# Optimization experiments

Measured on AMD Instinct MI355X. Metric: run time of the kernel, lower is better.

Reference implementation:

```python
import jax, jax.numpy as jnp
import numpy as np

N_POINTS = 131072
WIDTH = 256
DEPTH = 6          # number of hidden layers
MU = 1.0
K_COND = 0.5


def setup_inputs() -> dict:
    key = jax.random.key(0)
    ks = jax.random.split(key, 2 * (DEPTH + 1) + 1)
    xyt = jax.random.uniform(ks[0], (N_POINTS, 3), dtype=jnp.float32)
    dims = [3] + [WIDTH] * DEPTH + [1]
    inp = {"xyt": xyt}
    for i in range(DEPTH + 1):
        inp[f"w{i}"] = jax.random.normal(ks[1 + i], (dims[i], dims[i + 1]), dtype=jnp.float32) / np.sqrt(dims[i]).astype(np.float32)
        inp[f"b{i}"] = jnp.zeros((dims[i + 1],), dtype=jnp.float32)
    return inp


def reference(xyt, w0, b0, w1, b1, w2, b2, w3, b3, w4, b4, w5, b5, w6, b6):
    Ws = [w0, w1, w2, w3, w4, w5, w6]
    bs = [b0, b1, b2, b3, b4, b5, b6]

    def h_fn(p):  # p: (3,) -> scalar h(x,y,t)
        z = p
        for W, b in zip(Ws[:-1], bs[:-1]):
            z = jnp.tanh(z @ W + b)
        return (z @ Ws[-1] + bs[-1])[0]

    grad_h = jax.grad(h_fn)
    ex = jnp.array([1.0, 0.0, 0.0], dtype=xyt.dtype)
    ey = jnp.array([0.0, 1.0, 0.0], dtype=xyt.dtype)

    def point(p):
        h, g = jax.value_and_grad(h_fn)(p)          # h, (h_x, h_y, h_t)
        hxx = jax.jvp(grad_h, (p,), (ex,))[1][0]    # fwd-over-rev HVP, x-direction
        hyy = jax.jvp(grad_h, (p,), (ey,))[1][1]    # fwd-over-rev HVP, y-direction
        return h, g[0], g[1], g[2], hxx, hyy

    h, hx, hy, ht, hxx, hyy = jax.vmap(point)(xyt)  # each (n,)

    x, y, t = xyt[:, 0], xyt[:, 1], xyt[:, 2]
    f = jnp.sin(jnp.pi * x) * jnp.sin(jnp.pi * y) * jnp.exp(-t)  # problem.f

    res = MU * ht - K_COND * (h * (hxx + hyy) + hx * hx + hy * hy) - f
    return res[:, None]  # (n, 1)
```

## Files before the change

kernel.cpp:

```cpp
#include <hip/hip_runtime.h>
#include <math.h>

#define WIDTH 256
#define PTS 16
#define CPLANE 20480

typedef _Float16 f16x8 __attribute__((ext_vector_type(8)));
typedef _Float16 f16x4 __attribute__((ext_vector_type(4)));
typedef __fp16   h16x2 __attribute__((ext_vector_type(2)));
typedef float    f32x4 __attribute__((ext_vector_type(4)));

__device__ __forceinline__ void split2(float f, _Float16& h, _Float16& l) {
    h = (_Float16)f;
    l = (_Float16)(f - (float)h);
}
__device__ __forceinline__ void tanh_s(float u, float& z, float& s) {
    const float t = __expf(-2.0f * fabsf(u));
    const float r = __builtin_amdgcn_rcpf(1.0f + t);
    const float zm = (1.0f - t) * r;
    z = copysignf(zm, u);
    s = 4.0f * t * r * r;
}

__global__ void prep_w_kernel(const float* __restrict__ w1, const float* __restrict__ w2,
                              const float* __restrict__ w3, const float* __restrict__ w4,
                              const float* __restrict__ w5, _Float16* __restrict__ wt2)
{
    const int idx = blockIdx.x * blockDim.x + threadIdx.x;
    if (idx >= 5 * 16 * 8 * 64) return;
    const int lane = idx & 63;
    const int kc   = (idx >> 6) & 7;
    const int jt   = (idx >> 9) & 15;
    const int l    = idx >> 13;
    const float* Wsrc[5] = { w1, w2, w3, w4, w5 };
    const float* W = Wsrc[l];
    const int j  = jt * 16 + (lane & 15);
    const int k0 = kc * 32 + (lane >> 4) * 8;
    f16x8 vh, vl;
    #pragma unroll
    for (int i = 0; i < 8; ++i) {
        _Float16 h, lo;
        split2(W[(k0 + i) * WIDTH + j], h, lo);
        vh[i] = h; vl[i] = lo;
    }
    const int fo = ((jt * 8 + kc) * 64 + lane) * 8;
    *(f16x8*)(wt2 + (l * 2 + 0) * 65536 + fo) = vh;
    *(f16x8*)(wt2 + (l * 2 + 1) * 65536 + fo) = vl;
}

__global__ __launch_bounds__(256, 2)
void pde_mfma_kernel(const float* __restrict__ xyt,
                     const float* __restrict__ w0, const float* __restrict__ b0,
                     const float* __restrict__ b1, const float* __restrict__ b2,
                     const float* __restrict__ b3, const float* __restrict__ b4,
                     const float* __restrict__ b5,
                     const float* __restrict__ w6, const float* __restrict__ b6,
                     const _Float16* __restrict__ wt2,
                     float* __restrict__ out)
{
    __shared__ _Float16 Zs[CPLANE];
    float* redf = (float*)Zs;

    const int tid = threadIdx.x;
    const long gp0 = (long)blockIdx.x * PTS;

    {
        const int p = tid & 15;
        const float x = xyt[(gp0 + p) * 3 + 0];
        const float y = xyt[(gp0 + p) * 3 + 1];
        const float t = xyt[(gp0 + p) * 3 + 2];
        #pragma unroll
        for (int half = 0; half < 2; ++half) {
            const int jg = (tid >> 4) + half * 16;
            f16x8 vh[5];
            #pragma unroll
            for (int c = 0; c < 8; ++c) {
                const int j = jg * 8 + c;
                const float wx = w0[0 * WIDTH + j];
                const float wy = w0[1 * WIDTH + j];
                const float wt = w0[2 * WIDTH + j];
                float zv, s;
                tanh_s(fmaf(x, wx, fmaf(y, wy, fmaf(t, wt, b0[j]))), zv, s);
                const float vals[5] = { zv, s * wx, s * wy, s * wt,
                                        -2.0f * zv * s * (wx * wx + wy * wy) };
                #pragma unroll
                for (int v = 0; v < 5; ++v)
                    vh[v][c] = (_Float16)vals[v];
            }
            #pragma unroll
            for (int v = 0; v < 5; ++v) {
                const int off = ((v * 8 + (jg >> 2)) * 64 + (jg & 3) * 16 + p) * 8;
                *(f16x8*)&Zs[off] = vh[v];
            }
        }
    }
    __syncthreads();

    const float* Bsl[5] = { b1, b2, b3, b4, b5 };
    const int lane = tid & 63;
    const int wv   = tid >> 6;
    const int q    = lane >> 4;
    const int n15  = lane & 15;

    for (int l = 0; l < 5; ++l) {
        const _Float16* Wl = wt2 + l * 2 * 65536;
        f32x4 acc[5][4];
        #pragma unroll
        for (int v = 0; v < 5; ++v)
            #pragma unroll
            for (int Mt = 0; Mt < 4; ++Mt)
                acc[v][Mt] = (f32x4){0.f, 0.f, 0.f, 0.f};

        #pragma unroll 2
        for (int kc = 0; kc < 8; ++kc) {
            f16x8 Ah[4];
            #pragma unroll
            for (int Mt = 0; Mt < 4; ++Mt) {
                const int fo = (((wv * 4 + Mt) * 8 + kc) * 64 + lane) * 8;
                Ah[Mt] = *(const f16x8*)(Wl + fo);
            }
            #pragma unroll
            for (int v = 0; v < 5; ++v) {
                const int zo = ((v * 8 + kc) * 64 + lane) * 8;
                const f16x8 Bh = *(const f16x8*)&Zs[zo];
                #pragma unroll
                for (int Mt = 0; Mt < 4; ++Mt)
                    acc[v][Mt] = __builtin_amdgcn_mfma_f32_16x16x32_f16(
                                     Ah[Mt], Bh, acc[v][Mt], 0, 0, 0);
            }
        }
        __syncthreads();

        const float* Bb = Bsl[l];
        if (l < 4) {
            #pragma unroll
            for (int Mt = 0; Mt < 4; ++Mt) {
                const int jt = wv * 4 + Mt;
                float nv[5][4];
                #pragma unroll
                for (int reg = 0; reg < 4; ++reg) {
                    const int j = jt * 16 + q * 4 + reg;
                    float zv, s;
                    tanh_s(acc[0][Mt][reg] + Bb[j], zv, s);
                    const float u1 = acc[1][Mt][reg];
                    const float u2 = acc[2][Mt][reg];
                    nv[0][reg] = zv;
                    nv[1][reg] = s * u1;
                    nv[2][reg] = s * u2;
                    nv[3][reg] = s * acc[3][Mt][reg];
                    nv[4][reg] = fmaf(-2.0f * zv * s, fmaf(u1, u1, u2 * u2),
                                      s * acc[4][Mt][reg]);
                }
                const int j0 = jt * 16 + q * 4;
                const int off0 = ((j0 >> 5) * 64 + ((j0 >> 3) & 3) * 16 + n15) * 8 + (j0 & 7);
                #pragma unroll
                for (int v = 0; v < 5; ++v) {
                    const h16x2 h01 = __builtin_amdgcn_cvt_pkrtz(nv[v][0], nv[v][1]);
                    const h16x2 h23 = __builtin_amdgcn_cvt_pkrtz(nv[v][2], nv[v][3]);
                    *(f16x4*)&Zs[v * 4096 + off0] =
                        (f16x4){ (_Float16)h01[0], (_Float16)h01[1],
                                 (_Float16)h23[0], (_Float16)h23[1] };
                }
            }
        } else {
            float part[5] = {0.f, 0.f, 0.f, 0.f, 0.f};
            #pragma unroll
            for (int Mt = 0; Mt < 4; ++Mt) {
                const int jt = wv * 4 + Mt;
                #pragma unroll
                for (int reg = 0; reg < 4; ++reg) {
                    const int j = jt * 16 + q * 4 + reg;
                    float zv, s;
                    tanh_s(acc[0][Mt][reg] + Bb[j], zv, s);
                    const float u1 = acc[1][Mt][reg];
                    const float u2 = acc[2][Mt][reg];
                    const float w6j = w6[j];
                    part[0] = fmaf(zv, w6j, part[0]);
                    part[1] = fmaf(s * u1, w6j, part[1]);
                    part[2] = fmaf(s * u2, w6j, part[2]);
                    part[3] = fmaf(s * acc[3][Mt][reg], w6j, part[3]);
                    part[4] = fmaf(fmaf(-2.0f * zv * s, fmaf(u1, u1, u2 * u2),
                                        s * acc[4][Mt][reg]), w6j, part[4]);
                }
            }
            #pragma unroll
            for (int v = 0; v < 5; ++v) {
                part[v] += __shfl_xor(part[v], 16, 64);
                part[v] += __shfl_xor(part[v], 32, 64);
            }
            if (q == 0) {
                #pragma unroll
                for (int v = 0; v < 5; ++v)
                    redf[wv * 80 + v * 16 + n15] = part[v];
            }
        }
        __syncthreads();
    }

    if (tid < PTS) {
        const int p = tid;
        float tot[5];
        #pragma unroll
        for (int v = 0; v < 5; ++v)
            tot[v] = redf[0 * 80 + v * 16 + p] + redf[1 * 80 + v * 16 + p]
                   + redf[2 * 80 + v * 16 + p] + redf[3 * 80 + v * 16 + p];
        const float h   = tot[0] + b6[0];
        const float hx  = tot[1];
        const float hy  = tot[2];
        const float ht  = tot[3];
        const float lap = tot[4];
        const float x = xyt[(gp0 + p) * 3 + 0];
        const float y = xyt[(gp0 + p) * 3 + 1];
        const float t = xyt[(gp0 + p) * 3 + 2];
        const float pi = 3.14159265358979323846f;
        const float f = sinf(pi * x) * sinf(pi * y) * expf(-t);
        out[gp0 + p] = ht - 0.5f * (fmaf(h, lap, fmaf(hx, hx, hy * hy))) - f;
    }
}

extern "C" void kernel_launch(void* const* d_in, const int* in_sizes, int n_in,
                              void* d_out, int out_size, void* d_ws, size_t ws_size,
                              hipStream_t stream) {
    const float* xyt = (const float*)d_in[0];
    const float* w0  = (const float*)d_in[1];
    const float* b0  = (const float*)d_in[2];
    const float* w1  = (const float*)d_in[3];
    const float* b1  = (const float*)d_in[4];
    const float* w2  = (const float*)d_in[5];
    const float* b2  = (const float*)d_in[6];
    const float* w3  = (const float*)d_in[7];
    const float* b3  = (const float*)d_in[8];
    const float* w4  = (const float*)d_in[9];
    const float* b4  = (const float*)d_in[10];
    const float* w5  = (const float*)d_in[11];
    const float* b5  = (const float*)d_in[12];
    const float* w6  = (const float*)d_in[13];
    const float* b6  = (const float*)d_in[14];
    float* out = (float*)d_out;
    _Float16* wt2 = (_Float16*)d_ws;

    prep_w_kernel<<<160, 256, 0, stream>>>(w1, w2, w3, w4, w5, wt2);

    const int npts = in_sizes[0] / 3;
    dim3 grid(npts / PTS);
    dim3 block(256);
    pde_mfma_kernel<<<grid, block, 0, stream>>>(xyt, w0, b0, b1, b2, b3, b4, b5,
                                                w6, b6, wt2, out);
}
```

Measured before the change: 503.3 us.

## Raise occupancy target, vectorize epilogue math and bias loads, simplify tanh

Raises the launch-bounds minimum blocks per SM from 2 to 4, which pushes the compiler to keep register use lower so more waves can be resident. The tanh helper now clamps its input instead of using fabs and copysign. The layer epilogues are rewritten with float4 vector arithmetic and vectorized bias and w6 loads, and layer 0 loads w0 and b0 as float4. The tighter register budget may cause spills in the MFMA loop with its large accumulator set.

```diff
diff --git a/kernel.cpp b/kernel.cpp
--- a/kernel.cpp
+++ b/kernel.cpp
@@ -15,10 +15,10 @@
     l = (_Float16)(f - (float)h);
 }
 __device__ __forceinline__ void tanh_s(float u, float& z, float& s) {
-    const float t = __expf(-2.0f * fabsf(u));
+    const float uc = fminf(9.0f, fmaxf(-9.0f, u));
+    const float t = __expf(-2.0f * uc);
     const float r = __builtin_amdgcn_rcpf(1.0f + t);
-    const float zm = (1.0f - t) * r;
-    z = copysignf(zm, u);
+    z = (1.0f - t) * r;
     s = 4.0f * t * r * r;
 }
 
@@ -48,7 +48,7 @@
     *(f16x8*)(wt2 + (l * 2 + 1) * 65536 + fo) = vl;
 }
 
-__global__ __launch_bounds__(256, 2)
+__global__ __launch_bounds__(256, 4)
 void pde_mfma_kernel(const float* __restrict__ xyt,
                      const float* __restrict__ w0, const float* __restrict__ b0,
                      const float* __restrict__ b1, const float* __restrict__ b2,
@@ -74,18 +74,23 @@
             const int jg = (tid >> 4) + half * 16;
             f16x8 vh[5];
             #pragma unroll
-            for (int c = 0; c < 8; ++c) {
-                const int j = jg * 8 + c;
-                const float wx = w0[0 * WIDTH + j];
-                const float wy = w0[1 * WIDTH + j];
-                const float wt = w0[2 * WIDTH + j];
-                float zv, s;
-                tanh_s(fmaf(x, wx, fmaf(y, wy, fmaf(t, wt, b0[j]))), zv, s);
-                const float vals[5] = { zv, s * wx, s * wy, s * wt,
-                                        -2.0f * zv * s * (wx * wx + wy * wy) };
-                #pragma unroll
-                for (int v = 0; v < 5; ++v)
-                    vh[v][c] = (_Float16)vals[v];
+            for (int cb = 0; cb < 2; ++cb) {
+                const int jb = jg * 8 + cb * 4;
+                const f32x4 wx4 = *(const f32x4*)&w0[0 * WIDTH + jb];
+                const f32x4 wy4 = *(const f32x4*)&w0[1 * WIDTH + jb];
+                const f32x4 wt4 = *(const f32x4*)&w0[2 * WIDTH + jb];
+                const f32x4 bb4 = *(const f32x4*)&b0[jb];
+                #pragma unroll
+                for (int c = 0; c < 4; ++c) {
+                    const float wx = wx4[c], wy = wy4[c], wt = wt4[c];
+                    float zv, s;
+                    tanh_s(fmaf(x, wx, fmaf(y, wy, fmaf(t, wt, bb4[c]))), zv, s);
+                    const float vals[5] = { zv, s * wx, s * wy, s * wt,
+                                            -2.0f * zv * s * (wx * wx + wy * wy) };
+                    #pragma unroll
+                    for (int v = 0; v < 5; ++v)
+                        vh[v][cb * 4 + c] = (_Float16)vals[v];
+                }
             }
             #pragma unroll
             for (int v = 0; v < 5; ++v) {
@@ -136,55 +141,63 @@
             #pragma unroll
             for (int Mt = 0; Mt < 4; ++Mt) {
                 const int jt = wv * 4 + Mt;
-                float nv[5][4];
+                const int j0 = jt * 16 + q * 4;
+                const f32x4 bb = *(const f32x4*)&Bb[j0];
+                f32x4 zv, sv;
                 #pragma unroll
                 for (int reg = 0; reg < 4; ++reg) {
-                    const int j = jt * 16 + q * 4 + reg;
-                    float zv, s;
-                    tanh_s(acc[0][Mt][reg] + Bb[j], zv, s);
-                    const float u1 = acc[1][Mt][reg];
-                    const float u2 = acc[2][Mt][reg];
-                    nv[0][reg] = zv;
-                    nv[1][reg] = s * u1;
-                    nv[2][reg] = s * u2;
-                    nv[3][reg] = s * acc[3][Mt][reg];
-                    nv[4][reg] = fmaf(-2.0f * zv * s, fmaf(u1, u1, u2 * u2),
-                                      s * acc[4][Mt][reg]);
-                }
-                const int j0 = jt * 16 + q * 4;
+                    float z_, s_;
+                    tanh_s(acc[0][Mt][reg] + bb[reg], z_, s_);
+                    zv[reg] = z_; sv[reg] = s_;
+                }
+                const f32x4 u1 = acc[1][Mt], u2 = acc[2][Mt];
+                const f32x4 nv1 = sv * u1;
+                const f32x4 nv2 = sv * u2;
+                const f32x4 nv3 = sv * acc[3][Mt];
+                const f32x4 m2zs = -2.0f * zv * sv;
+                const f32x4 qq = u1 * u1 + u2 * u2;
+                const f32x4 nv4 = sv * acc[4][Mt] + m2zs * qq;
+                const f32x4 nvs[5] = { zv, nv1, nv2, nv3, nv4 };
                 const int off0 = ((j0 >> 5) * 64 + ((j0 >> 3) & 3) * 16 + n15) * 8 + (j0 & 7);
                 #pragma unroll
                 for (int v = 0; v < 5; ++v) {
-                    const h16x2 h01 = __builtin_amdgcn_cvt_pkrtz(nv[v][0], nv[v][1]);
-                    const h16x2 h23 = __builtin_amdgcn_cvt_pkrtz(nv[v][2], nv[v][3]);
+                    const h16x2 h01 = __builtin_amdgcn_cvt_pkrtz(nvs[v][0], nvs[v][1]);
+                    const h16x2 h23 = __builtin_amdgcn_cvt_pkrtz(nvs[v][2], nvs[v][3]);
                     *(f16x4*)&Zs[v * 4096 + off0] =
                         (f16x4){ (_Float16)h01[0], (_Float16)h01[1],
                                  (_Float16)h23[0], (_Float16)h23[1] };
                 }
             }
         } else {
-            float part[5] = {0.f, 0.f, 0.f, 0.f, 0.f};
+            f32x4 pv[5];
+            #pragma unroll
+            for (int v = 0; v < 5; ++v) pv[v] = (f32x4){0.f, 0.f, 0.f, 0.f};
             #pragma unroll
             for (int Mt = 0; Mt < 4; ++Mt) {
                 const int jt = wv * 4 + Mt;
+                const int j0 = jt * 16 + q * 4;
+                const f32x4 bb  = *(const f32x4*)&Bb[j0];
+                const f32x4 w64 = *(const f32x4*)&w6[j0];
+                f32x4 zv, sv;
                 #pragma unroll
                 for (int reg = 0; reg < 4; ++reg) {
-                    const int j = jt * 16 + q * 4 + reg;
-                    float zv, s;
-                    tanh_s(acc[0][Mt][reg] + Bb[j], zv, s);
-                    const float u1 = acc[1][Mt][reg];
-                    const float u2 = acc[2][Mt][reg];
-                    const float w6j = w6[j];
-                    part[0] = fmaf(zv, w6j, part[0]);
-                    part[1] = fmaf(s * u1, w6j, part[1]);
-                    part[2] = fmaf(s * u2, w6j, part[2]);
-                    part[3] = fmaf(s * acc[3][Mt][reg], w6j, part[3]);
-                    part[4] = fmaf(fmaf(-2.0f * zv * s, fmaf(u1, u1, u2 * u2),
-                                        s * acc[4][Mt][reg]), w6j, part[4]);
-                }
-            }
+                    float z_, s_;
+                    tanh_s(acc[0][Mt][reg] + bb[reg], z_, s_);
+                    zv[reg] = z_; sv[reg] = s_;
+                }
+                const f32x4 u1 = acc[1][Mt], u2 = acc[2][Mt];
+                const f32x4 m2zs = -2.0f * zv * sv;
+                const f32x4 qq = u1 * u1 + u2 * u2;
+                pv[0] += zv * w64;
+                pv[1] += (sv * u1) * w64;
+                pv[2] += (sv * u2) * w64;
+                pv[3] += (sv * acc[3][Mt]) * w64;
+                pv[4] += (sv * acc[4][Mt] + m2zs * qq) * w64;
+            }
+            float part[5];
             #pragma unroll
             for (int v = 0; v < 5; ++v) {
+                part[v] = (pv[v][0] + pv[v][1]) + (pv[v][2] + pv[v][3]);
                 part[v] += __shfl_xor(part[v], 16, 64);
                 part[v] += __shfl_xor(part[v], 32, 64);
             }
```

New measurement: 513.9 us (median of 2 runs). 1.02x slower.
